# Kernel optimization log

Hardware: AMD Instinct MI355X
Metric: run time of the kernel (lower is better)

The kernel has to match this reference:

```python
import jax, jax.numpy as jnp
import numpy as np

EPS = 1e-7  # keras backend epsilon

def setup_inputs() -> dict:
    key = jax.random.key(0)
    k1, k2, k3, k4, k5 = jax.random.split(key, 5)
    B, S, D, A = 64, 2048, 512, 256
    x = jax.random.normal(k1, (B, S, D), dtype=jnp.float32)
    mask = jax.random.randint(k2, (B, S), 0, 2) > 0
    # keras 'normal' initializer: RandomNormal(stddev=0.05)
    W = 0.05 * jax.random.normal(k3, (D, A), dtype=jnp.float32)
    b = 0.05 * jax.random.normal(k4, (A,), dtype=jnp.float32)
    u = 0.05 * jax.random.normal(k5, (A, 1), dtype=jnp.float32)
    return {"x": x, "mask": mask, "W": W, "b": b, "u": u}

def reference(x, mask, W, b, u):
    # x: [B,S,D], W: [D,A], b: [A], u: [A,1]
    uit = jnp.tanh(jnp.einsum('bsd,da->bsa', x, W) + b)   # [B,S,A]
    ait = jnp.einsum('bsa,a->bs', uit, u[:, 0])           # [B,S]
    ait = jnp.exp(ait)
    ait = ait * mask.astype(x.dtype)
    ait = ait / (jnp.sum(ait, axis=1, keepdims=True) + EPS)  # [B,S]
    return jnp.einsum('bsd,bs->bd', x, ait)               # [B,D]
```

## Files before the change

### kernel.cpp

```cpp
#include <hip/hip_runtime.h>
#include <stdint.h>

#define B_ 64
#define S_ 2048
#define D_ 512
#define A_ 256
#define TM 32
#define NTILES 64
#define EPS 1e-7f

typedef short bf16x8 __attribute__((ext_vector_type(8)));
typedef float f32x4  __attribute__((ext_vector_type(4)));

#define WS_WT   0
#define WS_NUM  262144
#define WS_Z    393216
#define WS_FLAG 393472

__device__ __forceinline__ uint32_t f32pair_to_bf16(float a, float b) {
  uint32_t ua = __float_as_uint(a), ub = __float_as_uint(b);
  ua = (ua + 0x7fffu + ((ua >> 16) & 1u)) >> 16;
  ub = (ub + 0x7fffu + ((ub >> 16) & 1u)) & 0xffff0000u;
  return ua | ub;
}

__global__ __launch_bounds__(256) void prep_kernel(
    const float* __restrict__ W, const void* __restrict__ mask,
    uint16_t* __restrict__ Wt, float* __restrict__ num,
    float* __restrict__ Z, int* __restrict__ flag)
{
  int i = blockIdx.x * 256 + threadIdx.x;
  if (i < A_ * D_) {
    int a = i >> 9;
    int d = i & (D_ - 1);
    uint32_t u = __float_as_uint(W[d * A_ + a]);
    u = (u + 0x7fffu + ((u >> 16) & 1u)) >> 16;
    Wt[i] = (uint16_t)u;
  } else if (i < A_ * D_ + B_ * D_) {
    num[i - A_ * D_] = 0.0f;
  } else if (i < A_ * D_ + B_ * D_ + B_) {
    Z[i - A_ * D_ - B_ * D_] = 0.0f;
  }
  if (blockIdx.x == 0 && threadIdx.x < 64) {
    const uint32_t* mw = (const uint32_t*)mask;
    int hit = 0;
    for (int k = 0; k < 16; ++k) {
      uint32_t v = mw[threadIdx.x + 64 * k];
      uint32_t b0 = v & 0xff, b1 = (v >> 8) & 0xff, b2 = (v >> 16) & 0xff, b3 = v >> 24;
      if (b0 <= 1u && b1 <= 1u && b2 <= 1u && b3 <= 1u && (b1 | b2 | b3)) hit = 1;
    }
    hit = __any(hit);
    if (threadIdx.x == 0) *flag = hit ? 1 : 0;
  }
}

__global__ __launch_bounds__(256, 4) void att_main(
    const float* __restrict__ x, const void* __restrict__ mask,
    const float* __restrict__ bias, const float* __restrict__ uvec,
    const uint16_t* __restrict__ Wt, float* __restrict__ num,
    float* __restrict__ Z, const int* __restrict__ flag)
{
  __shared__ uint16_t xs[TM * D_];
  __shared__ float sp[4][TM];
  __shared__ float ev[TM];

  const int tid  = threadIdx.x;
  const int bx   = blockIdx.x;
  const int b    = bx >> 6;
  const int tile = bx & 63;
  const int s0   = tile * TM;

  const float* xb = x + ((size_t)b * S_ + (size_t)s0) * D_;
  #pragma unroll
  for (int half = 0; half < 2; ++half) {
    float4 v[4][2];
    #pragma unroll
    for (int c = 0; c < 4; ++c) {
      int p   = (half * 4 + c) * 256 + tid;
      int row = p >> 6;
      int ch  = p & 63;
      const float* src = xb + row * D_ + ch * 8;
      v[c][0] = *(const float4*)(src);
      v[c][1] = *(const float4*)(src + 4);
    }
    #pragma unroll
    for (int c = 0; c < 4; ++c) {
      int p   = (half * 4 + c) * 256 + tid;
      int row = p >> 6;
      int ch  = p & 63;
      uint4 pk;
      pk.x = f32pair_to_bf16(v[c][0].x, v[c][0].y);
      pk.y = f32pair_to_bf16(v[c][0].z, v[c][0].w);
      pk.z = f32pair_to_bf16(v[c][1].x, v[c][1].y);
      pk.w = f32pair_to_bf16(v[c][1].z, v[c][1].w);
      int cc = ch ^ (row & 7);
      *(uint4*)(&xs[row * D_ + cc * 8]) = pk;
    }
  }
  __syncthreads();

  const int l  = tid & 63;
  const int w  = tid >> 6;
  const int lr = l & 15;
  const int lg = l >> 4;

  f32x4 acc[2][4];
  #pragma unroll
  for (int mt = 0; mt < 2; ++mt)
    #pragma unroll
    for (int nt = 0; nt < 4; ++nt)
      acc[mt][nt] = (f32x4){0.f, 0.f, 0.f, 0.f};

  const uint16_t* WtBase = Wt + (size_t)(w * 64 + lr) * D_;

  #pragma unroll 4
  for (int ks = 0; ks < 16; ++ks) {
    bf16x8 af[2], bfr[4];
    #pragma unroll
    for (int mt = 0; mt < 2; ++mt) {
      int row = mt * 16 + lr;
      int cc  = (ks * 4 + lg) ^ (lr & 7);
      af[mt]  = *(const bf16x8*)(&xs[row * D_ + cc * 8]);
    }
    #pragma unroll
    for (int nt = 0; nt < 4; ++nt)
      bfr[nt] = *(const bf16x8*)(WtBase + nt * 16 * D_ + ks * 32 + lg * 8);
    #pragma unroll
    for (int mt = 0; mt < 2; ++mt)
      #pragma unroll
      for (int nt = 0; nt < 4; ++nt)
        acc[mt][nt] = __builtin_amdgcn_mfma_f32_16x16x32_bf16(af[mt], bfr[nt], acc[mt][nt], 0, 0, 0);
  }

  float bn[4], un[4];
  #pragma unroll
  for (int nt = 0; nt < 4; ++nt) {
    int n = w * 64 + nt * 16 + lr;
    bn[nt] = bias[n];
    un[nt] = uvec[n];
  }
  #pragma unroll
  for (int mt = 0; mt < 2; ++mt) {
    #pragma unroll
    for (int r = 0; r < 4; ++r) {
      float ssum = 0.0f;
      #pragma unroll
      for (int nt = 0; nt < 4; ++nt) {
        float v  = acc[mt][nt][r] + bn[nt];
        float av = fabsf(v);
        float e2 = __expf(-2.0f * av);
        float t  = 1.0f - 2.0f * e2 * __builtin_amdgcn_rcpf(1.0f + e2);
        ssum += copysignf(t, v) * un[nt];
      }
      ssum += __shfl_xor(ssum, 1);
      ssum += __shfl_xor(ssum, 2);
      ssum += __shfl_xor(ssum, 4);
      ssum += __shfl_xor(ssum, 8);
      if (lr == 0) sp[w][mt * 16 + lg * 4 + r] = ssum;
    }
  }
  __syncthreads();

  if (tid < TM) {
    float score = sp[0][tid] + sp[1][tid] + sp[2][tid] + sp[3][tid];
    int midx = b * S_ + s0 + tid;
    int mval;
    if (*flag) mval = ((const unsigned char*)mask)[midx] != 0;
    else       mval = ((const int*)mask)[midx] != 0;
    float e = mval ? __expf(score) : 0.0f;
    ev[tid] = e;
    float tot = e;
    #pragma unroll
    for (int o = 1; o < TM; o <<= 1) tot += __shfl_xor(tot, o);
    if (tid == 0) atomicAdd(&Z[b], tot);
  }
  __syncthreads();

  {
    int d0 = tid * 2;
    int c0 = d0 >> 3;
    int j  = d0 & 7;
    float a0 = 0.0f, a1 = 0.0f;
    #pragma unroll 8
    for (int s = 0; s < TM; ++s) {
      int cc = c0 ^ (s & 7);
      uint32_t v = *(const uint32_t*)(&xs[s * D_ + cc * 8 + j]);
      float e = ev[s];
      a0 = fmaf(e, __uint_as_float(v << 16), a0);
      a1 = fmaf(e, __uint_as_float(v & 0xffff0000u), a1);
    }
    atomicAdd(&num[b * D_ + d0], a0);
    atomicAdd(&num[b * D_ + d0 + 1], a1);
  }
}

__global__ __launch_bounds__(256) void scale_kernel(
    const float* __restrict__ num, const float* __restrict__ Z,
    float* __restrict__ out)
{
  int idx = blockIdx.x * 256 + threadIdx.x;
  int b = idx >> 9;
  out[idx] = num[idx] / (Z[b] + EPS);
}

extern "C" void kernel_launch(void* const* d_in, const int* in_sizes, int n_in,
                              void* d_out, int out_size, void* d_ws, size_t ws_size,
                              hipStream_t stream)
{
  const float* x    = (const float*)d_in[0];
  const void*  mask = d_in[1];
  const float* W    = (const float*)d_in[2];
  const float* bias = (const float*)d_in[3];
  const float* u    = (const float*)d_in[4];
  float* out = (float*)d_out;

  char* ws = (char*)d_ws;
  uint16_t* Wt  = (uint16_t*)(ws + WS_WT);
  float* num    = (float*)(ws + WS_NUM);
  float* Z      = (float*)(ws + WS_Z);
  int*   flag   = (int*)(ws + WS_FLAG);

  int prep_threads = A_ * D_ + B_ * D_ + B_;
  prep_kernel<<<(prep_threads + 255) / 256, 256, 0, stream>>>(W, mask, Wt, num, Z, flag);
  att_main<<<B_ * NTILES, 256, 0, stream>>>(x, mask, bias, u, Wt, num, Z, flag);
  scale_kernel<<<(B_ * D_ + 255) / 256, 256, 0, stream>>>(num, Z, out);
}
```

Measured before the change: 445.2 us.

## Make attention kernel persistent with register-resident W and double-buffered x tiles

Replaces the 4096 short-lived blocks with 256 blocks of 512 threads. Each block loops over 16 sequence tiles, keeps its slice of the bf16 W matrix in registers, and double-buffers x tiles in LDS with a register prefetch of the next tile. Per-block partial numerators and Z are written to workspace and reduced in the scale kernel, which removes the global atomics and the zero-init pass. The cost is heavy register pressure from 32 bf16x8 fragments, and with only 256 blocks the GPU may be undersubscribed while the loop stays serialized by three barriers per tile.

```diff
diff --git a/kernel.cpp b/kernel.cpp
--- a/kernel.cpp
+++ b/kernel.cpp
@@ -6,16 +6,17 @@
 #define D_ 512
 #define A_ 256
 #define TM 32
-#define NTILES 64
+#define TPB 16
+#define NBLK 256
 #define EPS 1e-7f
 
 typedef short bf16x8 __attribute__((ext_vector_type(8)));
 typedef float f32x4  __attribute__((ext_vector_type(4)));
 
 #define WS_WT   0
-#define WS_NUM  262144
-#define WS_Z    393216
-#define WS_FLAG 393472
+#define WS_PART 262144
+#define WS_ZP   786432
+#define WS_FLAG 787456
 
 __device__ __forceinline__ uint32_t f32pair_to_bf16(float a, float b) {
   uint32_t ua = __float_as_uint(a), ub = __float_as_uint(b);
@@ -26,8 +27,7 @@
 
 __global__ __launch_bounds__(256) void prep_kernel(
     const float* __restrict__ W, const void* __restrict__ mask,
-    uint16_t* __restrict__ Wt, float* __restrict__ num,
-    float* __restrict__ Z, int* __restrict__ flag)
+    uint16_t* __restrict__ Wt, int* __restrict__ flag)
 {
   int i = blockIdx.x * 256 + threadIdx.x;
   if (i < A_ * D_) {
@@ -36,10 +36,6 @@
     uint32_t u = __float_as_uint(W[d * A_ + a]);
     u = (u + 0x7fffu + ((u >> 16) & 1u)) >> 16;
     Wt[i] = (uint16_t)u;
-  } else if (i < A_ * D_ + B_ * D_) {
-    num[i - A_ * D_] = 0.0f;
-  } else if (i < A_ * D_ + B_ * D_ + B_) {
-    Z[i - A_ * D_ - B_ * D_] = 0.0f;
   }
   if (blockIdx.x == 0 && threadIdx.x < 64) {
     const uint32_t* mw = (const uint32_t*)mask;
@@ -54,153 +50,169 @@
   }
 }
 
-__global__ __launch_bounds__(256, 4) void att_main(
+__global__ __launch_bounds__(512, 2) void att_main(
     const float* __restrict__ x, const void* __restrict__ mask,
     const float* __restrict__ bias, const float* __restrict__ uvec,
-    const uint16_t* __restrict__ Wt, float* __restrict__ num,
-    float* __restrict__ Z, const int* __restrict__ flag)
-{
-  __shared__ uint16_t xs[TM * D_];
-  __shared__ float sp[4][TM];
+    const uint16_t* __restrict__ Wt, float* __restrict__ part,
+    float* __restrict__ Zpart, const int* __restrict__ flag)
+{
+  __shared__ uint16_t xs[2][TM * D_];
+  __shared__ float sp[8][TM];
   __shared__ float ev[TM];
 
-  const int tid  = threadIdx.x;
-  const int bx   = blockIdx.x;
-  const int b    = bx >> 6;
-  const int tile = bx & 63;
-  const int s0   = tile * TM;
-
-  const float* xb = x + ((size_t)b * S_ + (size_t)s0) * D_;
+  const int tid = threadIdx.x;
+  const int l  = tid & 63, w  = tid >> 6;
+  const int lr = l & 15,   lg = l >> 4;
+  const int bx = blockIdx.x;
+  const int b  = bx >> 2;
+  const int s0 = (bx & 3) * (TM * TPB);
+  const float* xb = x + ((size_t)b * S_ + s0) * D_;
+  const int mflag = *flag;
+
+  bf16x8 bfr[32];
+  {
+    const uint16_t* wtb = Wt + (size_t)(w * 32 + lr) * D_;
+    #pragma unroll
+    for (int ks = 0; ks < 16; ++ks)
+      #pragma unroll
+      for (int nt = 0; nt < 2; ++nt)
+        bfr[ks * 2 + nt] = *(const bf16x8*)(wtb + nt * 16 * D_ + ks * 32 + lg * 8);
+  }
+  float bn[2], un[2];
   #pragma unroll
-  for (int half = 0; half < 2; ++half) {
-    float4 v[4][2];
+  for (int nt = 0; nt < 2; ++nt) {
+    int n = w * 32 + nt * 16 + lr;
+    bn[nt] = bias[n];
+    un[nt] = uvec[n];
+  }
+
+  float num_acc = 0.0f;
+  float zacc    = 0.0f;
+
+  float4 v[4][2];
+  #pragma unroll
+  for (int c = 0; c < 4; ++c) {
+    int q = c * 512 + tid;
+    const float* src = xb + (q >> 6) * D_ + (q & 63) * 8;
+    v[c][0] = *(const float4*)src;
+    v[c][1] = *(const float4*)(src + 4);
+  }
+
+  for (int t = 0; t < TPB; ++t) {
+    uint16_t* buf = xs[t & 1];
+
     #pragma unroll
     for (int c = 0; c < 4; ++c) {
-      int p   = (half * 4 + c) * 256 + tid;
-      int row = p >> 6;
-      int ch  = p & 63;
-      const float* src = xb + row * D_ + ch * 8;
-      v[c][0] = *(const float4*)(src);
-      v[c][1] = *(const float4*)(src + 4);
-    }
-    #pragma unroll
-    for (int c = 0; c < 4; ++c) {
-      int p   = (half * 4 + c) * 256 + tid;
-      int row = p >> 6;
-      int ch  = p & 63;
+      int q = c * 512 + tid;
+      int row = q >> 6, cb = q & 63;
       uint4 pk;
       pk.x = f32pair_to_bf16(v[c][0].x, v[c][0].y);
       pk.y = f32pair_to_bf16(v[c][0].z, v[c][0].w);
       pk.z = f32pair_to_bf16(v[c][1].x, v[c][1].y);
       pk.w = f32pair_to_bf16(v[c][1].z, v[c][1].w);
-      int cc = ch ^ (row & 7);
-      *(uint4*)(&xs[row * D_ + cc * 8]) = pk;
-    }
-  }
-  __syncthreads();
-
-  const int l  = tid & 63;
-  const int w  = tid >> 6;
-  const int lr = l & 15;
-  const int lg = l >> 4;
-
-  f32x4 acc[2][4];
-  #pragma unroll
-  for (int mt = 0; mt < 2; ++mt)
-    #pragma unroll
-    for (int nt = 0; nt < 4; ++nt)
-      acc[mt][nt] = (f32x4){0.f, 0.f, 0.f, 0.f};
-
-  const uint16_t* WtBase = Wt + (size_t)(w * 64 + lr) * D_;
-
-  #pragma unroll 4
-  for (int ks = 0; ks < 16; ++ks) {
-    bf16x8 af[2], bfr[4];
+      *(uint4*)(&buf[row * D_ + (cb ^ (row & 7)) * 8]) = pk;
+    }
+    __syncthreads();
+
+    if (t + 1 < TPB) {
+      const float* xt = xb + (size_t)(t + 1) * TM * D_;
+      #pragma unroll
+      for (int c = 0; c < 4; ++c) {
+        int q = c * 512 + tid;
+        const float* src = xt + (q >> 6) * D_ + (q & 63) * 8;
+        v[c][0] = *(const float4*)src;
+        v[c][1] = *(const float4*)(src + 4);
+      }
+    }
+
+    f32x4 acc[2][2];
+    #pragma unroll
+    for (int mt = 0; mt < 2; ++mt)
+      #pragma unroll
+      for (int nt = 0; nt < 2; ++nt)
+        acc[mt][nt] = (f32x4){0.f, 0.f, 0.f, 0.f};
+
+    #pragma unroll
+    for (int ks = 0; ks < 16; ++ks) {
+      bf16x8 af[2];
+      #pragma unroll
+      for (int mt = 0; mt < 2; ++mt)
+        af[mt] = *(const bf16x8*)(&buf[(mt * 16 + lr) * D_ + (((ks * 4 + lg) ^ (lr & 7)) * 8)]);
+      #pragma unroll
+      for (int mt = 0; mt < 2; ++mt)
+        #pragma unroll
+        for (int nt = 0; nt < 2; ++nt)
+          acc[mt][nt] = __builtin_amdgcn_mfma_f32_16x16x32_bf16(af[mt], bfr[ks * 2 + nt], acc[mt][nt], 0, 0, 0);
+    }
+
     #pragma unroll
     for (int mt = 0; mt < 2; ++mt) {
-      int row = mt * 16 + lr;
-      int cc  = (ks * 4 + lg) ^ (lr & 7);
-      af[mt]  = *(const bf16x8*)(&xs[row * D_ + cc * 8]);
-    }
-    #pragma unroll
-    for (int nt = 0; nt < 4; ++nt)
-      bfr[nt] = *(const bf16x8*)(WtBase + nt * 16 * D_ + ks * 32 + lg * 8);
-    #pragma unroll
-    for (int mt = 0; mt < 2; ++mt)
-      #pragma unroll
-      for (int nt = 0; nt < 4; ++nt)
-        acc[mt][nt] = __builtin_amdgcn_mfma_f32_16x16x32_bf16(af[mt], bfr[nt], acc[mt][nt], 0, 0, 0);
-  }
-
-  float bn[4], un[4];
-  #pragma unroll
-  for (int nt = 0; nt < 4; ++nt) {
-    int n = w * 64 + nt * 16 + lr;
-    bn[nt] = bias[n];
-    un[nt] = uvec[n];
-  }
-  #pragma unroll
-  for (int mt = 0; mt < 2; ++mt) {
-    #pragma unroll
-    for (int r = 0; r < 4; ++r) {
-      float ssum = 0.0f;
-      #pragma unroll
-      for (int nt = 0; nt < 4; ++nt) {
-        float v  = acc[mt][nt][r] + bn[nt];
-        float av = fabsf(v);
-        float e2 = __expf(-2.0f * av);
-        float t  = 1.0f - 2.0f * e2 * __builtin_amdgcn_rcpf(1.0f + e2);
-        ssum += copysignf(t, v) * un[nt];
+      #pragma unroll
+      for (int r = 0; r < 4; ++r) {
+        float ssum = 0.0f;
+        #pragma unroll
+        for (int nt = 0; nt < 2; ++nt) {
+          float vv = acc[mt][nt][r] + bn[nt];
+          float av = fabsf(vv);
+          float e2 = __expf(-2.0f * av);
+          float th = 1.0f - 2.0f * e2 * __builtin_amdgcn_rcpf(1.0f + e2);
+          ssum += copysignf(th, vv) * un[nt];
+        }
+        ssum += __shfl_xor(ssum, 1);
+        ssum += __shfl_xor(ssum, 2);
+        ssum += __shfl_xor(ssum, 4);
+        ssum += __shfl_xor(ssum, 8);
+        if (lr == 0) sp[w][mt * 16 + lg * 4 + r] = ssum;
       }
-      ssum += __shfl_xor(ssum, 1);
-      ssum += __shfl_xor(ssum, 2);
-      ssum += __shfl_xor(ssum, 4);
-      ssum += __shfl_xor(ssum, 8);
-      if (lr == 0) sp[w][mt * 16 + lg * 4 + r] = ssum;
-    }
-  }
-  __syncthreads();
-
-  if (tid < TM) {
-    float score = sp[0][tid] + sp[1][tid] + sp[2][tid] + sp[3][tid];
-    int midx = b * S_ + s0 + tid;
-    int mval;
-    if (*flag) mval = ((const unsigned char*)mask)[midx] != 0;
-    else       mval = ((const int*)mask)[midx] != 0;
-    float e = mval ? __expf(score) : 0.0f;
-    ev[tid] = e;
-    float tot = e;
-    #pragma unroll
-    for (int o = 1; o < TM; o <<= 1) tot += __shfl_xor(tot, o);
-    if (tid == 0) atomicAdd(&Z[b], tot);
-  }
-  __syncthreads();
-
-  {
-    int d0 = tid * 2;
-    int c0 = d0 >> 3;
-    int j  = d0 & 7;
-    float a0 = 0.0f, a1 = 0.0f;
-    #pragma unroll 8
-    for (int s = 0; s < TM; ++s) {
-      int cc = c0 ^ (s & 7);
-      uint32_t v = *(const uint32_t*)(&xs[s * D_ + cc * 8 + j]);
-      float e = ev[s];
-      a0 = fmaf(e, __uint_as_float(v << 16), a0);
-      a1 = fmaf(e, __uint_as_float(v & 0xffff0000u), a1);
-    }
-    atomicAdd(&num[b * D_ + d0], a0);
-    atomicAdd(&num[b * D_ + d0 + 1], a1);
-  }
+    }
+    __syncthreads();
+
+    if (tid < TM) {
+      float score = 0.0f;
+      #pragma unroll
+      for (int ww = 0; ww < 8; ++ww) score += sp[ww][tid];
+      int midx = b * S_ + s0 + t * TM + tid;
+      int mv = mflag ? (((const unsigned char*)mask)[midx] != 0)
+                     : (((const int*)mask)[midx] != 0);
+      float e = mv ? __expf(score) : 0.0f;
+      ev[tid] = e;
+      float tot = e;
+      #pragma unroll
+      for (int o = 1; o < TM; o <<= 1) tot += __shfl_xor(tot, o);
+      if (tid == 0) zacc += tot;
+    }
+    __syncthreads();
+
+    {
+      int c = tid >> 3, wo = (tid & 7) >> 1;
+      #pragma unroll 8
+      for (int s = 0; s < TM; ++s) {
+        uint32_t vv = *(const uint32_t*)(&buf[s * D_ + (c ^ (s & 7)) * 8 + wo * 2]);
+        float xv = (tid & 1) ? __uint_as_float(vv & 0xffff0000u)
+                             : __uint_as_float(vv << 16);
+        num_acc = fmaf(ev[s], xv, num_acc);
+      }
+    }
+  }
+
+  part[(size_t)bx * D_ + tid] = num_acc;
+  if (tid == 0) Zpart[bx] = zacc;
 }
 
 __global__ __launch_bounds__(256) void scale_kernel(
-    const float* __restrict__ num, const float* __restrict__ Z,
+    const float* __restrict__ part, const float* __restrict__ Zpart,
     float* __restrict__ out)
 {
   int idx = blockIdx.x * 256 + threadIdx.x;
   int b = idx >> 9;
-  out[idx] = num[idx] / (Z[b] + EPS);
+  int d = idx & (D_ - 1);
+  float s = 0.0f, z = 0.0f;
+  #pragma unroll
+  for (int g = 0; g < 4; ++g) {
+    s += part[(size_t)(b * 4 + g) * D_ + d];
+    z += Zpart[b * 4 + g];
+  }
+  out[idx] = s / (z + EPS);
 }
 
 extern "C" void kernel_launch(void* const* d_in, const int* in_sizes, int n_in,
@@ -216,12 +228,11 @@
 
   char* ws = (char*)d_ws;
   uint16_t* Wt  = (uint16_t*)(ws + WS_WT);
-  float* num    = (float*)(ws + WS_NUM);
-  float* Z      = (float*)(ws + WS_Z);
+  float* part   = (float*)(ws + WS_PART);
+  float* Zpart  = (float*)(ws + WS_ZP);
   int*   flag   = (int*)(ws + WS_FLAG);
 
-  int prep_threads = A_ * D_ + B_ * D_ + B_;
-  prep_kernel<<<(prep_threads + 255) / 256, 256, 0, stream>>>(W, mask, Wt, num, Z, flag);
-  att_main<<<B_ * NTILES, 256, 0, stream>>>(x, mask, bias, u, Wt, num, Z, flag);
-  scale_kernel<<<(B_ * D_ + 255) / 256, 256, 0, stream>>>(num, Z, out);
-}
+  prep_kernel<<<(A_ * D_ + 255) / 256, 256, 0, stream>>>(W, mask, Wt, flag);
+  att_main<<<NBLK, 512, 0, stream>>>(x, mask, bias, u, Wt, part, Zpart, flag);
+  scale_kernel<<<(B_ * D_ + 255) / 256, 256, 0, stream>>>(part, Zpart, out);
+}
```

Measured after the change: 379.0 us. -14.9%, faster.
